# Optimization experiments

Hardware: AMD Instinct MI355X
Metric: run time of the kernel (lower is better)

The kernel has to match this reference:

```python
import jax, jax.numpy as jnp
import numpy as np

MARGIN = 0.3
NEG_FILL = 1e9  # larger than any real distance; keeps min-reduction valid


def setup_inputs() -> dict:
    key = jax.random.key(0)
    k1, k2 = jax.random.split(key)
    embeddings = jax.random.normal(k1, (4096, 256), dtype=jnp.float32)
    labels = jax.random.randint(k2, (4096,), 0, 512, dtype=jnp.int64)
    return {"embeddings": embeddings, "labels": labels}


def _pairwise_distances(embeddings):
    # Faithful to the torch version, including the zero-distance sqrt guard.
    dot = jnp.matmul(embeddings, embeddings.T)          # [B, B]
    sq = jnp.diagonal(dot)                              # [B]
    d2 = sq[None, :] - 2.0 * dot + sq[:, None]
    d2 = jnp.maximum(d2, 0.0)
    zero_mask = (d2 == 0.0).astype(embeddings.dtype)
    d = jnp.sqrt(d2 + zero_mask * 1e-16)
    return d * (1.0 - zero_mask)


def reference(embeddings, labels):
    B = labels.shape[0]
    d = _pairwise_distances(embeddings)                 # [B, B]

    same = labels[:, None] == labels[None, :]           # [B, B]
    eye = jnp.eye(B, dtype=bool)
    pos_mask = same & ~eye
    neg_mask = ~same

    has_pos = jnp.any(pos_mask, axis=1)
    has_neg = jnp.any(neg_mask, axis=1)
    valid = has_pos & has_neg                           # [B]

    # Row-wise masked reductions (distances >= 0 so -1 is a safe max fill).
    hardest_pos = jnp.max(jnp.where(pos_mask, d, -1.0), axis=1)
    hardest_neg = jnp.min(jnp.where(neg_mask, d, NEG_FILL), axis=1)

    per_anchor = jnp.maximum(hardest_pos - hardest_neg + MARGIN, 0.0)
    n_valid = jnp.sum(valid.astype(jnp.float32))
    total = jnp.sum(jnp.where(valid, per_anchor, 0.0))
    return jnp.where(n_valid > 0, total / jnp.maximum(n_valid, 1.0), 0.0)
```

## Files before the change

### kernel.cpp

```cpp
#include <hip/hip_runtime.h>
#include <hip/hip_fp16.h>

#define BN 4096
#define DIM 256
#define NBLK 32
#define NPAIR 528
#define NSLOT 32
#define MARGIN_F 0.3f
#define NEG_FILL_F 1e9f
#define HP_SENT_BITS 0xBF800000

typedef __attribute__((ext_vector_type(8))) _Float16 f16x8;
typedef __attribute__((ext_vector_type(4))) float f32x4;

__device__ __forceinline__ void gld_lds16(const void* g, void* l) {
    __builtin_amdgcn_global_load_lds(
        (const __attribute__((address_space(1))) unsigned int*)g,
        (__attribute__((address_space(3))) unsigned int*)l, 16, 0, 0);
}

__global__ __launch_bounds__(256) void tl_prep(const float* __restrict__ E,
                                               float* __restrict__ norms,
                                               float* __restrict__ red,
                                               ushort* __restrict__ Eh) {
    const int tid  = threadIdx.x;
    const int lane = tid & 63;
    const int row  = blockIdx.x * 4 + (tid >> 6);

    float4 v = reinterpret_cast<const float4*>(E + (size_t)row * DIM)[lane];
    float f[4] = {v.x, v.y, v.z, v.w};
    ushort hb[4];
    float s = 0.0f;
    #pragma unroll
    for (int q = 0; q < 4; ++q) {
        s += f[q] * f[q];
        hb[q] = __half_as_ushort(__float2half(f[q]));
    }
    const int kc = lane >> 1, half = lane & 1;
    const size_t co = (((size_t)(kc * BN + row)) << 3) + (size_t)(half * 4);
    *reinterpret_cast<ushort4*>(Eh + co) = make_ushort4(hb[0], hb[1], hb[2], hb[3]);

    #pragma unroll
    for (int m = 32; m; m >>= 1) s += __shfl_xor(s, m, 64);
    if (lane == 0) norms[row] = s;
    if (blockIdx.x == 0 && tid < 3) red[tid] = 0.0f;
}

__global__ __launch_bounds__(256) void tl_main(const ushort* __restrict__ Eh,
                                               const int* __restrict__ labels,
                                               const float* __restrict__ norms,
                                               float* __restrict__ pHP,
                                               float* __restrict__ pHN) {
    __shared__ __align__(16) ushort smem[65536];

    const int tid  = threadIdx.x;
    const int lane = tid & 63;
    const int wave = tid >> 6;
    const int wy = wave >> 1, wx = wave & 1;
    const int quad = lane >> 4, l15 = lane & 15;

    int t = blockIdx.x, ib = 0, off = 0;
    while (off + (NBLK - ib) <= t) { off += NBLK - ib; ++ib; }
    const int jb = ib + (t - off);
    const int i0 = ib * 128, j0 = jb * 128;

    #pragma unroll
    for (int s = 0; s < 32; ++s) {
        const int idx  = s * 256 + tid;
        const int part = idx >> 12;
        const int kc   = (idx >> 7) & 31;
        const int m    = idx & 127;
        const int base = part ? j0 : i0;
        const ushort* src = Eh + (((size_t)(kc * BN + base + m)) << 3);
        gld_lds16(src, &smem[idx << 3]);
    }
    __syncthreads();

    f32x4 acc[4][4];
    #pragma unroll
    for (int r = 0; r < 4; ++r)
        #pragma unroll
        for (int c = 0; c < 4; ++c)
            acc[r][c] = (f32x4){0.f, 0.f, 0.f, 0.f};

    #pragma unroll
    for (int t8 = 0; t8 < 8; ++t8) {
        f16x8 a[4], b[4];
        #pragma unroll
        for (int r = 0; r < 4; ++r) {
            const int mi = wy * 64 + r * 16 + l15;
            a[r] = *reinterpret_cast<const f16x8*>(&smem[(((t8 * 4 + quad) * 128) + mi) * 8]);
        }
        #pragma unroll
        for (int c = 0; c < 4; ++c) {
            const int ni = wx * 64 + c * 16 + l15;
            b[c] = *reinterpret_cast<const f16x8*>(&smem[(32768 + ((t8 * 4 + quad) * 128 + ni) * 8)]);
        }
        #pragma unroll
        for (int c = 0; c < 4; ++c)
            #pragma unroll
            for (int r = 0; r < 4; ++r)
                acc[r][c] = __builtin_amdgcn_mfma_f32_16x16x32_f16(a[r], b[c], acc[r][c], 0, 0, 0);
    }

    const int rowBase = i0 + wy * 64;
    const int colBase = j0 + wx * 64;

    float nrow[4][4]; int lrow[4][4];
    #pragma unroll
    for (int r = 0; r < 4; ++r)
        #pragma unroll
        for (int e = 0; e < 4; ++e) {
            const int g = rowBase + r * 16 + quad * 4 + e;
            nrow[r][e] = norms[g];
            lrow[r][e] = labels[g];
        }
    float ncol[4]; int lcol[4];
    #pragma unroll
    for (int c = 0; c < 4; ++c) {
        const int g = colBase + c * 16 + l15;
        ncol[c] = norms[g];
        lcol[c] = labels[g];
    }

    float rmax2[4][4], rmin2[4][4], cmax2[4], cmin2[4];
    #pragma unroll
    for (int r = 0; r < 4; ++r)
        #pragma unroll
        for (int e = 0; e < 4; ++e) { rmax2[r][e] = -1.0f; rmin2[r][e] = NEG_FILL_F; }
    #pragma unroll
    for (int c = 0; c < 4; ++c) { cmax2[c] = -1.0f; cmin2[c] = NEG_FILL_F; }

    #pragma unroll
    for (int c = 0; c < 4; ++c) {
        const int gcol = colBase + c * 16 + l15;
        #pragma unroll
        for (int r = 0; r < 4; ++r) {
            #pragma unroll
            for (int e = 0; e < 4; ++e) {
                const int grow = rowBase + r * 16 + quad * 4 + e;
                float d2 = fmaxf(nrow[r][e] + ncol[c] - 2.0f * acc[r][c][e], 0.0f);
                if (lrow[r][e] == lcol[c]) {
                    if (grow != gcol) {
                        rmax2[r][e] = fmaxf(rmax2[r][e], d2);
                        cmax2[c]    = fmaxf(cmax2[c], d2);
                    }
                } else {
                    rmin2[r][e] = fminf(rmin2[r][e], d2);
                    cmin2[c]    = fminf(cmin2[c], d2);
                }
            }
        }
    }

    #pragma unroll
    for (int m = 1; m <= 8; m <<= 1) {
        #pragma unroll
        for (int r = 0; r < 4; ++r)
            #pragma unroll
            for (int e = 0; e < 4; ++e) {
                rmax2[r][e] = fmaxf(rmax2[r][e], __shfl_xor(rmax2[r][e], m, 64));
                rmin2[r][e] = fminf(rmin2[r][e], __shfl_xor(rmin2[r][e], m, 64));
            }
    }
    #pragma unroll
    for (int m = 16; m <= 32; m <<= 1) {
        #pragma unroll
        for (int c = 0; c < 4; ++c) {
            cmax2[c] = fmaxf(cmax2[c], __shfl_xor(cmax2[c], m, 64));
            cmin2[c] = fminf(cmin2[c], __shfl_xor(cmin2[c], m, 64));
        }
    }

    int*      srhp = reinterpret_cast<int*>(&smem[0]);
    unsigned* srhn = reinterpret_cast<unsigned*>(srhp + 128);
    int*      schp = srhp + 256;
    unsigned* schn = reinterpret_cast<unsigned*>(srhp + 384);
    __syncthreads();
    if (tid < 128) {
        srhp[tid] = (int)HP_SENT_BITS;
        srhn[tid] = __float_as_uint(NEG_FILL_F);
        schp[tid] = (int)HP_SENT_BITS;
        schn[tid] = __float_as_uint(NEG_FILL_F);
    }
    __syncthreads();
    if (l15 == 0) {
        #pragma unroll
        for (int r = 0; r < 4; ++r)
            #pragma unroll
            for (int e = 0; e < 4; ++e) {
                const int lr = wy * 64 + r * 16 + quad * 4 + e;
                atomicMax(&srhp[lr], __float_as_int(rmax2[r][e]));
                atomicMin(&srhn[lr], __float_as_uint(rmin2[r][e]));
            }
    }
    if (quad == 0) {
        #pragma unroll
        for (int c = 0; c < 4; ++c) {
            const int lc = wx * 64 + c * 16 + l15;
            atomicMax(&schp[lc], __float_as_int(cmax2[c]));
            atomicMin(&schn[lc], __float_as_uint(cmin2[c]));
        }
    }
    __syncthreads();
    if (tid < 128) {
        const float rp = __int_as_float(srhp[tid]);
        const float rn = __uint_as_float(srhn[tid]);
        const float cp = __int_as_float(schp[tid]);
        const float cn = __uint_as_float(schn[tid]);
        if (ib == jb) {
            pHP[(size_t)jb * BN + i0 + tid] = fmaxf(rp, cp);
            pHN[(size_t)jb * BN + i0 + tid] = fminf(rn, cn);
        } else {
            pHP[(size_t)jb * BN + i0 + tid] = rp;
            pHN[(size_t)jb * BN + i0 + tid] = rn;
            pHP[(size_t)ib * BN + j0 + tid] = cp;
            pHN[(size_t)ib * BN + j0 + tid] = cn;
        }
    }
}

__global__ __launch_bounds__(256) void tl_reduce(const float* __restrict__ pHP,
                                                 const float* __restrict__ pHN,
                                                 float* __restrict__ red,
                                                 float* __restrict__ out) {
    const int i = blockIdx.x * 256 + threadIdx.x;
    float hp2 = -1.0f, hn2 = NEG_FILL_F;
    #pragma unroll
    for (int s = 0; s < NSLOT; ++s) {
        hp2 = fmaxf(hp2, pHP[(size_t)s * BN + i]);
        hn2 = fminf(hn2, pHN[(size_t)s * BN + i]);
    }
    const bool valid = (hp2 >= 0.0f) && (hn2 < NEG_FILL_F);
    const float hp = sqrtf(fmaxf(hp2, 0.0f));
    const float hn = sqrtf(hn2);
    const float per = fmaxf(hp - hn + MARGIN_F, 0.0f);
    float s_ = valid ? per : 0.0f;
    float c_ = valid ? 1.0f : 0.0f;
    #pragma unroll
    for (int m = 32; m; m >>= 1) {
        s_ += __shfl_xor(s_, m, 64);
        c_ += __shfl_xor(c_, m, 64);
    }
    __shared__ float as_[4], ac_[4];
    const int wid = threadIdx.x >> 6;
    if ((threadIdx.x & 63) == 0) { as_[wid] = s_; ac_[wid] = c_; }
    __syncthreads();
    if (threadIdx.x == 0) {
        const float S = as_[0] + as_[1] + as_[2] + as_[3];
        const float C = ac_[0] + ac_[1] + ac_[2] + ac_[3];
        atomicAdd(&red[0], S);
        atomicAdd(&red[1], C);
        __threadfence();
        const unsigned ticket = atomicAdd(reinterpret_cast<unsigned*>(&red[2]), 1u);
        if (ticket == gridDim.x - 1) {
            const float S2 = atomicAdd(&red[0], 0.0f);
            const float C2 = atomicAdd(&red[1], 0.0f);
            out[0] = (C2 > 0.0f) ? (S2 / fmaxf(C2, 1.0f)) : 0.0f;
        }
    }
}

extern "C" void kernel_launch(void* const* d_in, const int* in_sizes, int n_in,
                              void* d_out, int out_size, void* d_ws, size_t ws_size,
                              hipStream_t stream) {
    const float* E      = (const float*)d_in[0];
    const int*   labels = (const int*)d_in[1];

    float*  ws    = (float*)d_ws;
    float*  norms = ws;
    float*  red   = ws + 4096;
    float*  pHP   = ws + 8192;
    float*  pHN   = ws + 8192 + NSLOT * BN;
    ushort* Eh    = (ushort*)(ws + 8192 + 2 * NSLOT * BN);

    tl_prep<<<BN / 4, 256, 0, stream>>>(E, norms, red, Eh);
    tl_main<<<NPAIR, 256, 0, stream>>>(Eh, labels, norms, pHP, pHN);
    tl_reduce<<<BN / 256, 256, 0, stream>>>(pHP, pHN, red, (float*)d_out);
}
```

Baseline: 98.95 us.

## Persist main kernel over tile pairs with prefetch and A-tile reuse

```diff
diff --git a/kernel.cpp b/kernel.cpp
--- a/kernel.cpp
+++ b/kernel.cpp
@@ -6,6 +6,7 @@
 #define NBLK 32
 #define NPAIR 528
 #define NSLOT 32
+#define GRID_MAIN 256
 #define MARGIN_F 0.3f
 #define NEG_FILL_F 1e9f
 #define HP_SENT_BITS 0xBF800000
@@ -17,6 +18,12 @@
     __builtin_amdgcn_global_load_lds(
         (const __attribute__((address_space(1))) unsigned int*)g,
         (__attribute__((address_space(3))) unsigned int*)l, 16, 0, 0);
+}
+
+__device__ __forceinline__ void decode_pair(int t, int& ib, int& jb) {
+    int off = 0; ib = 0;
+    while (off + (NBLK - ib) <= t) { off += NBLK - ib; ++ib; }
+    jb = ib + (t - off);
 }
 
 __global__ __launch_bounds__(256) void tl_prep(const float* __restrict__ E,
@@ -38,7 +45,11 @@
     }
     const int kc = lane >> 1, half = lane & 1;
     const size_t co = (((size_t)(kc * BN + row)) << 3) + (size_t)(half * 4);
-    *reinterpret_cast<ushort4*>(Eh + co) = make_ushort4(hb[0], hb[1], hb[2], hb[3]);
+    const unsigned w0 = (unsigned)hb[0] | ((unsigned)hb[1] << 16);
+    const unsigned w1 = (unsigned)hb[2] | ((unsigned)hb[3] << 16);
+    unsigned* dst = reinterpret_cast<unsigned*>(Eh + co);
+    __builtin_nontemporal_store(w0, dst);
+    __builtin_nontemporal_store(w1, dst + 1);
 
     #pragma unroll
     for (int m = 32; m; m >>= 1) s += __shfl_xor(s, m, 64);
@@ -51,171 +62,191 @@
                                                const float* __restrict__ norms,
                                                float* __restrict__ pHP,
                                                float* __restrict__ pHN) {
-    __shared__ __align__(16) ushort smem[65536];
+    __shared__ __align__(16) ushort smA[32768];
+    __shared__ __align__(16) ushort smB[32768];
+    __shared__ int comb[512];
 
     const int tid  = threadIdx.x;
     const int lane = tid & 63;
     const int wave = tid >> 6;
     const int wy = wave >> 1, wx = wave & 1;
     const int quad = lane >> 4, l15 = lane & 15;
-
-    int t = blockIdx.x, ib = 0, off = 0;
-    while (off + (NBLK - ib) <= t) { off += NBLK - ib; ++ib; }
-    const int jb = ib + (t - off);
-    const int i0 = ib * 128, j0 = jb * 128;
-
-    #pragma unroll
-    for (int s = 0; s < 32; ++s) {
-        const int idx  = s * 256 + tid;
-        const int part = idx >> 12;
-        const int kc   = (idx >> 7) & 31;
-        const int m    = idx & 127;
-        const int base = part ? j0 : i0;
-        const ushort* src = Eh + (((size_t)(kc * BN + base + m)) << 3);
-        gld_lds16(src, &smem[idx << 3]);
-    }
-    __syncthreads();
-
-    f32x4 acc[4][4];
-    #pragma unroll
-    for (int r = 0; r < 4; ++r)
-        #pragma unroll
-        for (int c = 0; c < 4; ++c)
-            acc[r][c] = (f32x4){0.f, 0.f, 0.f, 0.f};
-
-    #pragma unroll
-    for (int t8 = 0; t8 < 8; ++t8) {
-        f16x8 a[4], b[4];
-        #pragma unroll
-        for (int r = 0; r < 4; ++r) {
-            const int mi = wy * 64 + r * 16 + l15;
-            a[r] = *reinterpret_cast<const f16x8*>(&smem[(((t8 * 4 + quad) * 128) + mi) * 8]);
-        }
+    const int bid  = blockIdx.x;
+    const int nmine = 2 + ((bid < NPAIR - 2 * GRID_MAIN) ? 1 : 0);
+
+    auto stageA = [&](int ib) {
+        #pragma unroll
+        for (int s = 0; s < 16; ++s) {
+            const int idx = s * 256 + tid;
+            const int kc = idx >> 7, m = idx & 127;
+            gld_lds16(Eh + (((size_t)(kc * BN + ib * 128 + m)) << 3), &smA[idx << 3]);
+        }
+    };
+    auto stageB = [&](int jb) {
+        #pragma unroll
+        for (int s = 0; s < 16; ++s) {
+            const int idx = s * 256 + tid;
+            const int kc = idx >> 7, m = idx & 127;
+            gld_lds16(Eh + (((size_t)(kc * BN + jb * 128 + m)) << 3), &smB[idx << 3]);
+        }
+    };
+
+    int curIb = -1;
+    for (int pi = 0; pi < nmine; ++pi) {
+        const int t = (pi < 2) ? (2 * bid + pi) : (2 * GRID_MAIN + bid);
+        int ib, jb; decode_pair(t, ib, jb);
+        const int i0 = ib * 128, j0 = jb * 128;
+
+        if (pi == 0) { stageA(ib); curIb = ib; stageB(jb); }
+        __syncthreads();
+
+        f32x4 acc[4][4];
+        #pragma unroll
+        for (int r = 0; r < 4; ++r)
+            #pragma unroll
+            for (int c = 0; c < 4; ++c)
+                acc[r][c] = (f32x4){0.f, 0.f, 0.f, 0.f};
+
+        #pragma unroll
+        for (int t8 = 0; t8 < 8; ++t8) {
+            f16x8 a[4], b[4];
+            #pragma unroll
+            for (int r = 0; r < 4; ++r) {
+                const int mi = wy * 64 + r * 16 + l15;
+                a[r] = *reinterpret_cast<const f16x8*>(&smA[(((t8 * 4 + quad) * 128) + mi) * 8]);
+            }
+            #pragma unroll
+            for (int c = 0; c < 4; ++c) {
+                const int ni = wx * 64 + c * 16 + l15;
+                b[c] = *reinterpret_cast<const f16x8*>(&smB[(((t8 * 4 + quad) * 128) + ni) * 8]);
+            }
+            #pragma unroll
+            for (int c = 0; c < 4; ++c)
+                #pragma unroll
+                for (int r = 0; r < 4; ++r)
+                    acc[r][c] = __builtin_amdgcn_mfma_f32_16x16x32_f16(a[r], b[c], acc[r][c], 0, 0, 0);
+        }
+        __syncthreads();
+
+        const int rowBase = i0 + wy * 64;
+        const int colBase = j0 + wx * 64;
+        float nrow[4][4]; int lrow[4][4];
+        #pragma unroll
+        for (int r = 0; r < 4; ++r)
+            #pragma unroll
+            for (int e = 0; e < 4; ++e) {
+                const int g = rowBase + r * 16 + quad * 4 + e;
+                nrow[r][e] = norms[g];
+                lrow[r][e] = labels[g];
+            }
+        float ncol[4]; int lcol[4];
         #pragma unroll
         for (int c = 0; c < 4; ++c) {
-            const int ni = wx * 64 + c * 16 + l15;
-            b[c] = *reinterpret_cast<const f16x8*>(&smem[(32768 + ((t8 * 4 + quad) * 128 + ni) * 8)]);
-        }
-        #pragma unroll
-        for (int c = 0; c < 4; ++c)
+            const int g = colBase + c * 16 + l15;
+            ncol[c] = norms[g];
+            lcol[c] = labels[g];
+        }
+
+        if (pi + 1 < nmine) {
+            const int tn = (pi + 1 < 2) ? (2 * bid + pi + 1) : (2 * GRID_MAIN + bid);
+            int ibn, jbn; decode_pair(tn, ibn, jbn);
+            if (ibn != curIb) { stageA(ibn); curIb = ibn; }
+            stageB(jbn);
+        }
+
+        float rmax2[4][4], rmin2[4][4], cmax2[4], cmin2[4];
+        #pragma unroll
+        for (int r = 0; r < 4; ++r)
+            #pragma unroll
+            for (int e = 0; e < 4; ++e) { rmax2[r][e] = -1.0f; rmin2[r][e] = NEG_FILL_F; }
+        #pragma unroll
+        for (int c = 0; c < 4; ++c) { cmax2[c] = -1.0f; cmin2[c] = NEG_FILL_F; }
+
+        #pragma unroll
+        for (int c = 0; c < 4; ++c) {
+            const int gcol = colBase + c * 16 + l15;
+            #pragma unroll
+            for (int r = 0; r < 4; ++r) {
+                #pragma unroll
+                for (int e = 0; e < 4; ++e) {
+                    const int grow = rowBase + r * 16 + quad * 4 + e;
+                    float d2 = fmaxf(nrow[r][e] + ncol[c] - 2.0f * acc[r][c][e], 0.0f);
+                    if (lrow[r][e] == lcol[c]) {
+                        if (grow != gcol) {
+                            rmax2[r][e] = fmaxf(rmax2[r][e], d2);
+                            cmax2[c]    = fmaxf(cmax2[c], d2);
+                        }
+                    } else {
+                        rmin2[r][e] = fminf(rmin2[r][e], d2);
+                        cmin2[c]    = fminf(cmin2[c], d2);
+                    }
+                }
+            }
+        }
+
+        #pragma unroll
+        for (int m = 1; m <= 8; m <<= 1) {
             #pragma unroll
             for (int r = 0; r < 4; ++r)
-                acc[r][c] = __builtin_amdgcn_mfma_f32_16x16x32_f16(a[r], b[c], acc[r][c], 0, 0, 0);
-    }
-
-    const int rowBase = i0 + wy * 64;
-    const int colBase = j0 + wx * 64;
-
-    float nrow[4][4]; int lrow[4][4];
-    #pragma unroll
-    for (int r = 0; r < 4; ++r)
-        #pragma unroll
-        for (int e = 0; e < 4; ++e) {
-            const int g = rowBase + r * 16 + quad * 4 + e;
-            nrow[r][e] = norms[g];
-            lrow[r][e] = labels[g];
-        }
-    float ncol[4]; int lcol[4];
-    #pragma unroll
-    for (int c = 0; c < 4; ++c) {
-        const int g = colBase + c * 16 + l15;
-        ncol[c] = norms[g];
-        lcol[c] = labels[g];
-    }
-
-    float rmax2[4][4], rmin2[4][4], cmax2[4], cmin2[4];
-    #pragma unroll
-    for (int r = 0; r < 4; ++r)
-        #pragma unroll
-        for (int e = 0; e < 4; ++e) { rmax2[r][e] = -1.0f; rmin2[r][e] = NEG_FILL_F; }
-    #pragma unroll
-    for (int c = 0; c < 4; ++c) { cmax2[c] = -1.0f; cmin2[c] = NEG_FILL_F; }
-
-    #pragma unroll
-    for (int c = 0; c < 4; ++c) {
-        const int gcol = colBase + c * 16 + l15;
-        #pragma unroll
-        for (int r = 0; r < 4; ++r) {
-            #pragma unroll
-            for (int e = 0; e < 4; ++e) {
-                const int grow = rowBase + r * 16 + quad * 4 + e;
-                float d2 = fmaxf(nrow[r][e] + ncol[c] - 2.0f * acc[r][c][e], 0.0f);
-                if (lrow[r][e] == lcol[c]) {
-                    if (grow != gcol) {
-                        rmax2[r][e] = fmaxf(rmax2[r][e], d2);
-                        cmax2[c]    = fmaxf(cmax2[c], d2);
-                    }
-                } else {
-                    rmin2[r][e] = fminf(rmin2[r][e], d2);
-                    cmin2[c]    = fminf(cmin2[c], d2);
+                #pragma unroll
+                for (int e = 0; e < 4; ++e) {
+                    rmax2[r][e] = fmaxf(rmax2[r][e], __shfl_xor(rmax2[r][e], m, 64));
+                    rmin2[r][e] = fminf(rmin2[r][e], __shfl_xor(rmin2[r][e], m, 64));
                 }
-            }
-        }
-    }
-
-    #pragma unroll
-    for (int m = 1; m <= 8; m <<= 1) {
-        #pragma unroll
-        for (int r = 0; r < 4; ++r)
-            #pragma unroll
-            for (int e = 0; e < 4; ++e) {
-                rmax2[r][e] = fmaxf(rmax2[r][e], __shfl_xor(rmax2[r][e], m, 64));
-                rmin2[r][e] = fminf(rmin2[r][e], __shfl_xor(rmin2[r][e], m, 64));
-            }
-    }
-    #pragma unroll
-    for (int m = 16; m <= 32; m <<= 1) {
-        #pragma unroll
-        for (int c = 0; c < 4; ++c) {
-            cmax2[c] = fmaxf(cmax2[c], __shfl_xor(cmax2[c], m, 64));
-            cmin2[c] = fminf(cmin2[c], __shfl_xor(cmin2[c], m, 64));
-        }
-    }
-
-    int*      srhp = reinterpret_cast<int*>(&smem[0]);
-    unsigned* srhn = reinterpret_cast<unsigned*>(srhp + 128);
-    int*      schp = srhp + 256;
-    unsigned* schn = reinterpret_cast<unsigned*>(srhp + 384);
-    __syncthreads();
-    if (tid < 128) {
-        srhp[tid] = (int)HP_SENT_BITS;
-        srhn[tid] = __float_as_uint(NEG_FILL_F);
-        schp[tid] = (int)HP_SENT_BITS;
-        schn[tid] = __float_as_uint(NEG_FILL_F);
-    }
-    __syncthreads();
-    if (l15 == 0) {
-        #pragma unroll
-        for (int r = 0; r < 4; ++r)
-            #pragma unroll
-            for (int e = 0; e < 4; ++e) {
-                const int lr = wy * 64 + r * 16 + quad * 4 + e;
-                atomicMax(&srhp[lr], __float_as_int(rmax2[r][e]));
-                atomicMin(&srhn[lr], __float_as_uint(rmin2[r][e]));
-            }
-    }
-    if (quad == 0) {
-        #pragma unroll
-        for (int c = 0; c < 4; ++c) {
-            const int lc = wx * 64 + c * 16 + l15;
-            atomicMax(&schp[lc], __float_as_int(cmax2[c]));
-            atomicMin(&schn[lc], __float_as_uint(cmin2[c]));
-        }
-    }
-    __syncthreads();
-    if (tid < 128) {
-        const float rp = __int_as_float(srhp[tid]);
-        const float rn = __uint_as_float(srhn[tid]);
-        const float cp = __int_as_float(schp[tid]);
-        const float cn = __uint_as_float(schn[tid]);
-        if (ib == jb) {
-            pHP[(size_t)jb * BN + i0 + tid] = fmaxf(rp, cp);
-            pHN[(size_t)jb * BN + i0 + tid] = fminf(rn, cn);
-        } else {
-            pHP[(size_t)jb * BN + i0 + tid] = rp;
-            pHN[(size_t)jb * BN + i0 + tid] = rn;
-            pHP[(size_t)ib * BN + j0 + tid] = cp;
-            pHN[(size_t)ib * BN + j0 + tid] = cn;
+        }
+        #pragma unroll
+        for (int m = 16; m <= 32; m <<= 1) {
+            #pragma unroll
+            for (int c = 0; c < 4; ++c) {
+                cmax2[c] = fmaxf(cmax2[c], __shfl_xor(cmax2[c], m, 64));
+                cmin2[c] = fminf(cmin2[c], __shfl_xor(cmin2[c], m, 64));
+            }
+        }
+
+        int*      srhp = comb;
+        unsigned* srhn = reinterpret_cast<unsigned*>(comb + 128);
+        int*      schp = comb + 256;
+        unsigned* schn = reinterpret_cast<unsigned*>(comb + 384);
+        if (tid < 128) {
+            srhp[tid] = (int)HP_SENT_BITS;
+            srhn[tid] = __float_as_uint(NEG_FILL_F);
+            schp[tid] = (int)HP_SENT_BITS;
+            schn[tid] = __float_as_uint(NEG_FILL_F);
+        }
+        __syncthreads();
+        if (l15 == 0) {
+            #pragma unroll
+            for (int r = 0; r < 4; ++r)
+                #pragma unroll
+                for (int e = 0; e < 4; ++e) {
+                    const int lr = wy * 64 + r * 16 + quad * 4 + e;
+                    atomicMax(&srhp[lr], __float_as_int(rmax2[r][e]));
+                    atomicMin(&srhn[lr], __float_as_uint(rmin2[r][e]));
+                }
+        }
+        if (quad == 0) {
+            #pragma unroll
+            for (int c = 0; c < 4; ++c) {
+                const int lc = wx * 64 + c * 16 + l15;
+                atomicMax(&schp[lc], __float_as_int(cmax2[c]));
+                atomicMin(&schn[lc], __float_as_uint(cmin2[c]));
+            }
+        }
+        __syncthreads();
+        if (tid < 128) {
+            const float rp = __int_as_float(srhp[tid]);
+            const float rn = __uint_as_float(srhn[tid]);
+            const float cp = __int_as_float(schp[tid]);
+            const float cn = __uint_as_float(schn[tid]);
+            if (ib == jb) {
+                pHP[(size_t)jb * BN + i0 + tid] = fmaxf(rp, cp);
+                pHN[(size_t)jb * BN + i0 + tid] = fminf(rn, cn);
+            } else {
+                pHP[(size_t)jb * BN + i0 + tid] = rp;
+                pHN[(size_t)jb * BN + i0 + tid] = rn;
+                pHP[(size_t)ib * BN + j0 + tid] = cp;
+                pHN[(size_t)ib * BN + j0 + tid] = cn;
+            }
         }
     }
 }
@@ -275,6 +306,6 @@
     ushort* Eh    = (ushort*)(ws + 8192 + 2 * NSLOT * BN);
 
     tl_prep<<<BN / 4, 256, 0, stream>>>(E, norms, red, Eh);
-    tl_main<<<NPAIR, 256, 0, stream>>>(Eh, labels, norms, pHP, pHN);
+    tl_main<<<GRID_MAIN, 256, 0, stream>>>(Eh, labels, norms, pHP, pHN);
     tl_reduce<<<BN / 256, 256, 0, stream>>>(pHP, pHN, red, (float*)d_out);
 }
```

Result: no change. 99.62 us (+0.7%).

## Double-buffer K-slabs through registers to overlap global loads with MFMA

Applied to the files above, without the earlier changes.

```diff
diff --git a/kernel.cpp b/kernel.cpp
--- a/kernel.cpp
+++ b/kernel.cpp
@@ -13,12 +13,6 @@
 typedef __attribute__((ext_vector_type(8))) _Float16 f16x8;
 typedef __attribute__((ext_vector_type(4))) float f32x4;
 
-__device__ __forceinline__ void gld_lds16(const void* g, void* l) {
-    __builtin_amdgcn_global_load_lds(
-        (const __attribute__((address_space(1))) unsigned int*)g,
-        (__attribute__((address_space(3))) unsigned int*)l, 16, 0, 0);
-}
-
 __global__ __launch_bounds__(256) void tl_prep(const float* __restrict__ E,
                                                float* __restrict__ norms,
                                                float* __restrict__ red,
@@ -51,7 +45,7 @@
                                                const float* __restrict__ norms,
                                                float* __restrict__ pHP,
                                                float* __restrict__ pHN) {
-    __shared__ __align__(16) ushort smem[65536];
+    __shared__ __align__(16) ushort smem[2][16384];
 
     const int tid  = threadIdx.x;
     const int lane = tid & 63;
@@ -64,17 +58,25 @@
     const int jb = ib + (t - off);
     const int i0 = ib * 128, j0 = jb * 128;
 
-    #pragma unroll
-    for (int s = 0; s < 32; ++s) {
-        const int idx  = s * 256 + tid;
-        const int part = idx >> 12;
-        const int kc   = (idx >> 7) & 31;
-        const int m    = idx & 127;
-        const int base = part ? j0 : i0;
-        const ushort* src = Eh + (((size_t)(kc * BN + base + m)) << 3);
-        gld_lds16(src, &smem[idx << 3]);
-    }
-    __syncthreads();
+    auto slab_load = [&](int kb, uint4* treg) {
+        #pragma unroll
+        for (int s = 0; s < 8; ++s) {
+            const int idx  = s * 256 + tid;
+            const int part = idx >> 10;
+            const int kc   = (idx >> 7) & 7;
+            const int m    = idx & 127;
+            const int base = part ? j0 : i0;
+            treg[s] = *reinterpret_cast<const uint4*>(
+                Eh + (((size_t)((kb * 8 + kc) * BN + base + m)) << 3));
+        }
+    };
+    auto slab_write = [&](int buf, const uint4* treg) {
+        #pragma unroll
+        for (int s = 0; s < 8; ++s) {
+            const int idx = s * 256 + tid;
+            *reinterpret_cast<uint4*>(&smem[buf][idx << 3]) = treg[s];
+        }
+    };
 
     f32x4 acc[4][4];
     #pragma unroll
@@ -83,24 +85,37 @@
         for (int c = 0; c < 4; ++c)
             acc[r][c] = (f32x4){0.f, 0.f, 0.f, 0.f};
 
-    #pragma unroll
-    for (int t8 = 0; t8 < 8; ++t8) {
-        f16x8 a[4], b[4];
-        #pragma unroll
-        for (int r = 0; r < 4; ++r) {
-            const int mi = wy * 64 + r * 16 + l15;
-            a[r] = *reinterpret_cast<const f16x8*>(&smem[(((t8 * 4 + quad) * 128) + mi) * 8]);
-        }
-        #pragma unroll
-        for (int c = 0; c < 4; ++c) {
-            const int ni = wx * 64 + c * 16 + l15;
-            b[c] = *reinterpret_cast<const f16x8*>(&smem[(32768 + ((t8 * 4 + quad) * 128 + ni) * 8)]);
-        }
-        #pragma unroll
-        for (int c = 0; c < 4; ++c)
-            #pragma unroll
-            for (int r = 0; r < 4; ++r)
-                acc[r][c] = __builtin_amdgcn_mfma_f32_16x16x32_f16(a[r], b[c], acc[r][c], 0, 0, 0);
+    uint4 treg[8];
+    slab_load(0, treg);
+    slab_write(0, treg);
+
+    #pragma unroll
+    for (int kb = 0; kb < DIM / 64; ++kb) {
+        const int buf = kb & 1;
+        if (kb + 1 < DIM / 64) slab_load(kb + 1, treg);
+        __syncthreads();
+
+        const ushort* sb = &smem[buf][0];
+        #pragma unroll
+        for (int h2 = 0; h2 < 2; ++h2) {
+            f16x8 a[4], b[4];
+            #pragma unroll
+            for (int r = 0; r < 4; ++r) {
+                const int mi = wy * 64 + r * 16 + l15;
+                a[r] = *reinterpret_cast<const f16x8*>(&sb[(((h2 * 4 + quad) * 128) + mi) * 8]);
+            }
+            #pragma unroll
+            for (int c = 0; c < 4; ++c) {
+                const int ni = wx * 64 + c * 16 + l15;
+                b[c] = *reinterpret_cast<const f16x8*>(&sb[((1024 + (h2 * 4 + quad) * 128) + ni) * 8]);
+            }
+            #pragma unroll
+            for (int c = 0; c < 4; ++c)
+                #pragma unroll
+                for (int r = 0; r < 4; ++r)
+                    acc[r][c] = __builtin_amdgcn_mfma_f32_16x16x32_f16(a[r], b[c], acc[r][c], 0, 0, 0);
+        }
+        if (kb + 1 < DIM / 64) slab_write(buf ^ 1, treg);
     }
 
     const int rowBase = i0 + wy * 64;
@@ -172,7 +187,7 @@
         }
     }
 
-    int*      srhp = reinterpret_cast<int*>(&smem[0]);
+    int*      srhp = reinterpret_cast<int*>(&smem[0][0]);
     unsigned* srhn = reinterpret_cast<unsigned*>(srhp + 128);
     int*      schp = srhp + 256;
     unsigned* schn = reinterpret_cast<unsigned*>(srhp + 384);
```

After: 107.1 us. +8.2%, slower.
